# Kernel tuning notes

Hardware: AMD Instinct MI355X
Metric: run time of the kernel (lower is better)

Reference implementation:

```python
import jax, jax.numpy as jnp
import numpy as np

# SMPL kinematic tree (24 joints)
PARENTS = [-1, 0, 0, 0, 1, 2, 3, 4, 5, 6, 7, 8, 9, 9, 9, 12, 13, 14, 16, 17, 18, 19, 20, 21]
B, V, J, NB = 1024, 6890, 24, 10
POSE_BASIS = 9 * (J - 1)  # 207


def setup_inputs() -> dict:
    key = jax.random.key(0)
    ks = jax.random.split(key, 8)
    betas = jax.random.normal(ks[0], (B, NB), jnp.float32)
    global_rot = jax.random.normal(ks[1], (B, 1, 3, 3), jnp.float32)
    body_pose = jax.random.normal(ks[2], (B, J - 1, 3, 3), jnp.float32)
    v_template = jax.random.normal(ks[3], (V, 3), jnp.float32)
    shapedirs = jax.random.normal(ks[4], (V, 3, NB), jnp.float32) * 0.01
    posedirs = jax.random.normal(ks[5], (POSE_BASIS, V * 3), jnp.float32) * 0.01
    J_regressor = jax.random.uniform(ks[6], (J, V), jnp.float32) / V
    w = jax.random.uniform(ks[7], (V, J), jnp.float32)
    lbs_weights = w / w.sum(-1, keepdims=True)
    return dict(betas=betas, global_rot=global_rot, body_pose=body_pose,
                v_template=v_template, shapedirs=shapedirs, posedirs=posedirs,
                J_regressor=J_regressor, lbs_weights=lbs_weights)


def reference(betas, global_rot, body_pose, v_template, shapedirs, posedirs,
              J_regressor, lbs_weights):
    b = betas.shape[0]
    full_pose = jnp.concatenate([global_rot, body_pose], axis=1)  # [B,24,3,3]

    # shape blend shapes
    v_shaped = v_template + jnp.einsum('bl,vcl->bvc', betas, shapedirs)  # [B,V,3]
    Jt = jnp.einsum('jv,bvc->bjc', J_regressor, v_shaped)  # [B,24,3]

    # pose blend shapes (pose2rot=False: rotations given)
    eye3 = jnp.eye(3, dtype=betas.dtype)
    pose_feature = (full_pose[:, 1:] - eye3).reshape(b, POSE_BASIS)  # [B,207]
    v_posed = v_shaped + (pose_feature @ posedirs).reshape(b, V, 3)

    # forward kinematics along parent chain
    rel_joints = jnp.concatenate(
        [Jt[:, :1], Jt[:, 1:] - Jt[:, jnp.array(PARENTS[1:])]], axis=1)  # [B,24,3]
    top = jnp.concatenate([full_pose, rel_joints[..., None]], axis=-1)  # [B,24,3,4]
    bottom = jnp.broadcast_to(jnp.array([0., 0., 0., 1.], dtype=betas.dtype),
                              (b, J, 1, 4))
    T_local = jnp.concatenate([top, bottom], axis=-2)  # [B,24,4,4]

    chain = [T_local[:, 0]]
    for i in range(1, J):  # fixed small tree, sequential dependency
        chain.append(chain[PARENTS[i]] @ T_local[:, i])
    A = jnp.stack(chain, axis=1)  # [B,24,4,4]

    posed_joints = A[..., :3, 3]  # [B,24,3]
    # make transforms relative to rest-pose joints
    rel_t = posed_joints - jnp.einsum('bjmn,bjn->bjm', A[..., :3, :3], Jt)
    A_rel = A.at[..., :3, 3].set(rel_t)

    # linear blend skinning
    T = jnp.einsum('vj,bjmn->bvmn', lbs_weights, A_rel)  # [B,V,4,4]
    vertices = jnp.einsum('bvmn,bvn->bvm', T[..., :3, :3], v_posed) + T[..., :3, 3]
    return vertices, posed_joints
```

## Files before the change

### kernel.cpp

```cpp
#include <hip/hip_runtime.h>

#define BN 1024
#define NV 6890
#define NBETA 10
#define PB 207
#define N3 20670
#define NCOL 20736
#define NCHUNK 7
#define BT 32

typedef __bf16 bf16x8 __attribute__((ext_vector_type(8)));
typedef float  f32x4  __attribute__((ext_vector_type(4)));

__device__ __constant__ int c_par[24] = {-1,0,0,0,1,2,3,4,5,6,7,8,9,9,9,12,13,14,16,17,18,19,20,21};

__device__ inline unsigned short f2bf(float f) {
    unsigned u = __float_as_uint(f);
    u += 0x7fff + ((u >> 16) & 1);
    return (unsigned short)(u >> 16);
}

__global__ __launch_bounds__(256) void k_prep(const float* __restrict__ pd,
                                              const float* __restrict__ sd,
                                              const float* __restrict__ vtm,
                                              const float* __restrict__ Jr,
                                              const float* __restrict__ bpose,
                                              const float* __restrict__ betas,
                                              const float* __restrict__ w,
                                              unsigned short* __restrict__ ws_pdt,
                                              unsigned short* __restrict__ ws_pfb,
                                              unsigned short* __restrict__ ws_wb,
                                              float* __restrict__ ws_jsp)
{
    int blk = blockIdx.x;
    if (blk < 567) {
        int t = blk * 256 + threadIdx.x;
        int kc = t / NCOL;
        int col = t - kc * NCOL;
        bool cok = col < N3;
        unsigned short vals[40];
        #pragma unroll
        for (int kk = 0; kk < 32; kk++) {
            int gk = kc * 32 + kk;
            float val = 0.f;
            if (cok) {
                if (gk < PB)             val = pd[(size_t)gk * N3 + col];
                else if (gk < PB + 10)   val = sd[(size_t)col * NBETA + (gk - PB)];
                else if (gk == PB + 10)  val = vtm[col];
            }
            vals[kk] = f2bf(val);
        }
        #pragma unroll
        for (int kk = 32; kk < 40; kk++) vals[kk] = 0;
        uint4* dst = (uint4*)(ws_pdt + (size_t)t * 40);
        #pragma unroll
        for (int q = 0; q < 5; q++) {
            uint4 u;
            u.x = vals[q*8+0] | ((unsigned)vals[q*8+1] << 16);
            u.y = vals[q*8+2] | ((unsigned)vals[q*8+3] << 16);
            u.z = vals[q*8+4] | ((unsigned)vals[q*8+5] << 16);
            u.w = vals[q*8+6] | ((unsigned)vals[q*8+7] << 16);
            dst[q] = u;
        }
    } else if (blk < 799) {
        int e0 = (blk - 567) * 1024 + threadIdx.x * 4;
        unsigned short v4[4];
        #pragma unroll
        for (int r = 0; r < 4; r++) {
            int e = e0 + r;
            int b = e / 232, k = e - b * 232;
            float x = 0.f;
            if (k < PB) {
                x = bpose[(size_t)b * PB + k];
                int k9 = k % 9;
                if (k9 == 0 || k9 == 4 || k9 == 8) x -= 1.f;
            } else if (k < PB + 10) {
                x = betas[b * NBETA + (k - PB)];
            } else if (k == PB + 10) {
                x = 1.f;
            }
            v4[r] = f2bf(x);
        }
        uint2 u;
        u.x = v4[0] | ((unsigned)v4[1] << 16);
        u.y = v4[2] | ((unsigned)v4[3] << 16);
        *(uint2*)(ws_pfb + e0) = u;
    } else if (blk < 1069) {
        int e0 = (blk - 799) * 1024 + threadIdx.x * 4;
        unsigned short v4[4];
        #pragma unroll
        for (int r = 0; r < 4; r++) {
            int e = e0 + r;
            int v = e / 40, j = e - v * 40;
            float val = (j < 24 && v < NV) ? w[(size_t)v * 24 + j] : 0.f;
            v4[r] = f2bf(val);
        }
        uint2 u;
        u.x = v4[0] | ((unsigned)v4[1] << 16);
        u.y = v4[2] | ((unsigned)v4[3] << 16);
        *(uint2*)(ws_wb + e0) = u;
    } else {
        int b2 = blk - 1069;
        int jc = b2 >> 3;
        int seg = b2 & 7;
        int j = jc / 3, c = jc % 3;
        int v0 = seg * 862;
        int v1 = v0 + 862; if (v1 > NV) v1 = NV;

        float acc[11];
        #pragma unroll
        for (int l = 0; l < 11; l++) acc[l] = 0.f;

        for (int v = v0 + threadIdx.x; v < v1; v += 256) {
            float r = Jr[j * NV + v];
            acc[10] += r * vtm[v * 3 + c];
            const float* s = sd + (size_t)(v * 3 + c) * NBETA;
            #pragma unroll
            for (int l = 0; l < NBETA; l++) acc[l] += r * s[l];
        }

        __shared__ float red[4][11];
        int lane = threadIdx.x & 63, wv = threadIdx.x >> 6;
        #pragma unroll
        for (int l = 0; l < 11; l++) {
            float x = acc[l];
            x += __shfl_down(x, 32, 64);
            x += __shfl_down(x, 16, 64);
            x += __shfl_down(x, 8, 64);
            x += __shfl_down(x, 4, 64);
            x += __shfl_down(x, 2, 64);
            x += __shfl_down(x, 1, 64);
            if (lane == 0) red[wv][l] = x;
        }
        __syncthreads();
        if (threadIdx.x == 0) {
            #pragma unroll
            for (int l = 0; l < 11; l++)
                ws_jsp[((size_t)seg * 72 + jc) * 11 + l]
                    = red[0][l] + red[1][l] + red[2][l] + red[3][l];
        }
    }
}

__global__ __launch_bounds__(256) void k_chain(const float* __restrict__ betas,
                                               const float* __restrict__ grot,
                                               const float* __restrict__ bpose,
                                               const float* __restrict__ ws_jsp,
                                               unsigned short* __restrict__ ws_artb,
                                               float* __restrict__ pj)
{
    __shared__ float js_s[72 * 11];
    __shared__ float jt[16][72];
    __shared__ float tl[16][288];
    __shared__ float am[16][288];
    int tid = threadIdx.x;

    for (int e = tid; e < 72 * 11; e += 256) {
        float s = 0.f;
        #pragma unroll
        for (int seg = 0; seg < 8; seg++)
            s += ws_jsp[(size_t)seg * 792 + e];
        js_s[e] = s;
    }
    __syncthreads();

    int lb = tid >> 4;
    int e  = tid & 15;
    int b  = blockIdx.x * 16 + lb;

    for (int idx = e; idx < 72; idx += 16) {
        float acc = js_s[idx * 11 + 10];
        const float* be = betas + b * NBETA;
        #pragma unroll
        for (int l = 0; l < NBETA; l++) acc += be[l] * js_s[idx * 11 + l];
        jt[lb][idx] = acc;
    }
    __syncthreads();

    for (int idx = e; idx < 288; idx += 16) {
        int j = idx / 12, e12 = idx % 12, m = e12 >> 2, n = e12 & 3;
        float val;
        if (n < 3) {
            val = (j == 0) ? grot[(size_t)b * 9 + m * 3 + n]
                           : bpose[((size_t)b * 23 + (j - 1)) * 9 + m * 3 + n];
        } else {
            val = jt[lb][j * 3 + m];
            if (j > 0) val -= jt[lb][c_par[j] * 3 + m];
        }
        tl[lb][idx] = val;
    }
    __syncthreads();

    if (e < 12) am[lb][e] = tl[lb][e];
    for (int i = 1; i < 24; i++) {
        __syncthreads();
        if (e < 12) {
            int p = c_par[i];
            int m = e >> 2, n = e & 3;
            float val = am[lb][p*12 + m*4 + 0] * tl[lb][i*12 + 0 + n]
                      + am[lb][p*12 + m*4 + 1] * tl[lb][i*12 + 4 + n]
                      + am[lb][p*12 + m*4 + 2] * tl[lb][i*12 + 8 + n];
            if (n == 3) val += am[lb][p*12 + m*4 + 3];
            am[lb][i*12 + e] = val;
        }
    }
    __syncthreads();

    for (int idx = e; idx < 72; idx += 16) {
        int j = idx / 3, m = idx % 3;
        pj[(size_t)b * 72 + idx] = am[lb][j*12 + m*4 + 3];
    }
    for (int idx = e; idx < 480; idx += 16) {
        int col = idx / 40, j = idx - col * 40;
        float val = 0.f;
        if (j < 24) {
            int m = col >> 2, n = col & 3;
            if (n < 3) {
                val = am[lb][j*12 + col];
            } else {
                val = am[lb][j*12 + m*4 + 3]
                    - am[lb][j*12 + m*4 + 0] * jt[lb][j*3 + 0]
                    - am[lb][j*12 + m*4 + 1] * jt[lb][j*3 + 1]
                    - am[lb][j*12 + m*4 + 2] * jt[lb][j*3 + 2];
            }
        }
        ws_artb[(size_t)b * 480 + idx] = f2bf(val);
    }
}

__global__ __launch_bounds__(256, 6) void k_vert(const unsigned short* __restrict__ ws_pdt,
                                                 const unsigned short* __restrict__ ws_pfb,
                                                 const unsigned short* __restrict__ ws_wb,
                                                 const unsigned short* __restrict__ ws_artb,
                                                 float* __restrict__ out)
{
    const int lin = blockIdx.x + 32 * blockIdx.y;
    const int xcd = lin & 7;
    const int loc = lin >> 3;
    const int g_id = xcd * 432 + loc;
    const int bb = g_id & 31;
    const int vb = g_id >> 5;

    const int tid = threadIdx.x;
    const int wv = tid >> 6;
    const int lane = tid & 63;
    const int r16 = lane & 15;
    const int half8 = (lane >> 4) * 8;

    __shared__ __align__(16) float disp_l[32 * 196];

    const unsigned short* pfbase = ws_pfb + (size_t)(bb * BT) * 232;
    const unsigned short* pB0 = ws_pdt + ((size_t)vb * 192 + wv * 48 + r16) * 40 + half8;

    bf16x8 a0 = *(const bf16x8*)(pfbase + r16 * 232 + half8);
    bf16x8 a1 = *(const bf16x8*)(pfbase + (16 + r16) * 232 + half8);
    bf16x8 b0 = *(const bf16x8*)(pB0);
    bf16x8 b1 = *(const bf16x8*)(pB0 + 640);
    bf16x8 b2 = *(const bf16x8*)(pB0 + 1280);

    f32x4 acc[2][3];
    #pragma unroll
    for (int mt = 0; mt < 2; mt++)
        #pragma unroll
        for (int t = 0; t < 3; t++)
            acc[mt][t] = (f32x4){0.f, 0.f, 0.f, 0.f};

    #pragma unroll
    for (int kc = 0; kc < NCHUNK; kc++) {
        bf16x8 a0n, a1n, b0n, b1n, b2n;
        if (kc < NCHUNK - 1) {
            const unsigned short* pn = pB0 + (size_t)(kc + 1) * NCOL * 40;
            b0n = *(const bf16x8*)(pn);
            b1n = *(const bf16x8*)(pn + 640);
            b2n = *(const bf16x8*)(pn + 1280);
            a0n = *(const bf16x8*)(pfbase + r16 * 232 + (kc + 1) * 32 + half8);
            a1n = *(const bf16x8*)(pfbase + (16 + r16) * 232 + (kc + 1) * 32 + half8);
        }
        acc[0][0] = __builtin_amdgcn_mfma_f32_16x16x32_bf16(a0, b0, acc[0][0], 0, 0, 0);
        acc[1][0] = __builtin_amdgcn_mfma_f32_16x16x32_bf16(a1, b0, acc[1][0], 0, 0, 0);
        acc[0][1] = __builtin_amdgcn_mfma_f32_16x16x32_bf16(a0, b1, acc[0][1], 0, 0, 0);
        acc[1][1] = __builtin_amdgcn_mfma_f32_16x16x32_bf16(a1, b1, acc[1][1], 0, 0, 0);
        acc[0][2] = __builtin_amdgcn_mfma_f32_16x16x32_bf16(a0, b2, acc[0][2], 0, 0, 0);
        acc[1][2] = __builtin_amdgcn_mfma_f32_16x16x32_bf16(a1, b2, acc[1][2], 0, 0, 0);
        if (kc < NCHUNK - 1) { a0 = a0n; a1 = a1n; b0 = b0n; b1 = b1n; b2 = b2n; }
    }

    #pragma unroll
    for (int mt = 0; mt < 2; mt++) {
        #pragma unroll
        for (int t = 0; t < 3; t++) {
            int col = wv * 48 + t * 16 + r16;
            int brow = mt * 16 + (lane >> 4) * 4;
            #pragma unroll
            for (int r = 0; r < 4; r++)
                disp_l[(brow + r) * 196 + col] = acc[mt][t][r];
        }
    }
    __syncthreads();

    bf16x8 aw = *(const bf16x8*)(ws_wb + (size_t)(vb * 64 + wv * 16 + r16) * 40 + half8);

    const int gq = lane >> 4;
    const int v16 = wv * 16 + r16;
    const int vg = vb * 64 + v16;
    int bl[3], mm[3];
    #pragma unroll
    for (int t = 0; t < 3; t++) {
        int q = 4 * t + gq;
        bl[t] = (q * 11) >> 5;
        mm[t] = q - 3 * bl[t];
    }

    const unsigned short* pArt = ws_artb + (size_t)(bb * BT) * 480 + (size_t)r16 * 40 + half8;

    bf16x8 c0 = *(const bf16x8*)(pArt);
    bf16x8 c1 = *(const bf16x8*)(pArt + 640);
    bf16x8 c2 = *(const bf16x8*)(pArt + 1280);

    #pragma unroll
    for (int sub = 0; sub < 8; sub++) {
        bf16x8 c0n, c1n, c2n;
        if (sub < 7) {
            const unsigned short* pn = pArt + (size_t)(sub + 1) * 1920;
            c0n = *(const bf16x8*)(pn);
            c1n = *(const bf16x8*)(pn + 640);
            c2n = *(const bf16x8*)(pn + 1280);
        }
        f32x4 z = (f32x4){0.f, 0.f, 0.f, 0.f};
        f32x4 t0 = __builtin_amdgcn_mfma_f32_16x16x32_bf16(c0, aw, z, 0, 0, 0);
        f32x4 t1 = __builtin_amdgcn_mfma_f32_16x16x32_bf16(c1, aw, z, 0, 0, 0);
        f32x4 t2 = __builtin_amdgcn_mfma_f32_16x16x32_bf16(c2, aw, z, 0, 0, 0);

        #pragma unroll
        for (int t = 0; t < 3; t++) {
            f32x4 tt = (t == 0) ? t0 : (t == 1) ? t1 : t2;
            int row = sub * 4 + bl[t];
            const float* d = disp_l + row * 196 + v16 * 3;
            float x = d[0], y = d[1], zz = d[2];
            float p = tt[0] * x + tt[1] * y + tt[2] * zz + tt[3];
            if (vg < NV)
                out[(size_t)(bb * BT + row) * N3 + (size_t)vg * 3 + mm[t]] = p;
        }
        if (sub < 7) { c0 = c0n; c1 = c1n; c2 = c2n; }
    }
}

extern "C" void kernel_launch(void* const* d_in, const int* in_sizes, int n_in,
                              void* d_out, int out_size, void* d_ws, size_t ws_size,
                              hipStream_t stream) {
    const float* betas = (const float*)d_in[0];
    const float* grot  = (const float*)d_in[1];
    const float* bpose = (const float*)d_in[2];
    const float* vtm   = (const float*)d_in[3];
    const float* sd    = (const float*)d_in[4];
    const float* pd    = (const float*)d_in[5];
    const float* Jr    = (const float*)d_in[6];
    const float* w     = (const float*)d_in[7];
    float* out = (float*)d_out;

    char* ws = (char*)d_ws;
    unsigned short* ws_pdt  = (unsigned short*)(ws);
    unsigned short* ws_pfb  = (unsigned short*)(ws + 11612160);
    unsigned short* ws_wb   = (unsigned short*)(ws + 12087296);
    float*          ws_jsp  = (float*)         (ws + 12640256);
    unsigned short* ws_artb = (unsigned short*)(ws + 12665600);

    k_prep<<<1645, 256, 0, stream>>>(pd, sd, vtm, Jr, bpose, betas, w,
                                     ws_pdt, ws_pfb, ws_wb, ws_jsp);
    k_chain<<<BN / 16, 256, 0, stream>>>(betas, grot, bpose, ws_jsp, ws_artb,
                                         out + (size_t)BN * N3);
    k_vert<<<dim3(32, 108), 256, 0, stream>>>(ws_pdt, ws_pfb, ws_wb, ws_artb, out);
}
```

Baseline: 185.6 us.

## Stage pose features in LDS via async DMA and re-split skinning across waves

The per-batch pose-feature tile is now copied into shared memory with global_load_lds DMA and read from LDS in the K loop, replacing per-wave global loads and register double-buffering. The skinning epilogue is re-partitioned so each wave handles two batch sub-blocks across all four vertex groups, rather than one vertex group across all eight sub-blocks. Occupancy hint drops from 6 to 4 blocks per CU to accommodate the larger LDS footprint. This aims to cut redundant global traffic for the A operand and the artb tiles, but adds a barrier and lowers occupancy. Output stores now come from each wave covering 64 vertices, which may change the coalescing pattern.

```diff
diff --git a/kernel.cpp b/kernel.cpp
--- a/kernel.cpp
+++ b/kernel.cpp
@@ -18,6 +18,12 @@
     unsigned u = __float_as_uint(f);
     u += 0x7fff + ((u >> 16) & 1);
     return (unsigned short)(u >> 16);
+}
+
+__device__ inline void dma16(const void* g, void* l) {
+    __builtin_amdgcn_global_load_lds(
+        (const __attribute__((address_space(1))) unsigned int*)g,
+        (__attribute__((address_space(3))) unsigned int*)l, 16, 0, 0);
 }
 
 __global__ __launch_bounds__(256) void k_prep(const float* __restrict__ pd,
@@ -228,7 +234,7 @@
     }
 }
 
-__global__ __launch_bounds__(256, 6) void k_vert(const unsigned short* __restrict__ ws_pdt,
+__global__ __launch_bounds__(256, 4) void k_vert(const unsigned short* __restrict__ ws_pdt,
                                                  const unsigned short* __restrict__ ws_pfb,
                                                  const unsigned short* __restrict__ ws_wb,
                                                  const unsigned short* __restrict__ ws_artb,
@@ -247,13 +253,19 @@
     const int r16 = lane & 15;
     const int half8 = (lane >> 4) * 8;
 
-    __shared__ __align__(16) float disp_l[32 * 196];
-
-    const unsigned short* pfbase = ws_pfb + (size_t)(bb * BT) * 232;
+    __shared__ __align__(16) unsigned char smem[40448];
+    float*          disp_l = (float*)smem;
+    unsigned short* pfb_l  = (unsigned short*)(smem + 25088);
+
+    {
+        const unsigned short* srcF = ws_pfb + (size_t)(bb * BT) * 232;
+        for (int i = wv; i < 14; i += 4)
+            dma16((const char*)srcF + i * 1024 + lane * 16, (char*)pfb_l + i * 1024);
+        if (wv == 2 && lane < 32)
+            dma16((const char*)srcF + 14 * 1024 + lane * 16, (char*)pfb_l + 14 * 1024);
+    }
+
     const unsigned short* pB0 = ws_pdt + ((size_t)vb * 192 + wv * 48 + r16) * 40 + half8;
-
-    bf16x8 a0 = *(const bf16x8*)(pfbase + r16 * 232 + half8);
-    bf16x8 a1 = *(const bf16x8*)(pfbase + (16 + r16) * 232 + half8);
     bf16x8 b0 = *(const bf16x8*)(pB0);
     bf16x8 b1 = *(const bf16x8*)(pB0 + 640);
     bf16x8 b2 = *(const bf16x8*)(pB0 + 1280);
@@ -265,16 +277,18 @@
         for (int t = 0; t < 3; t++)
             acc[mt][t] = (f32x4){0.f, 0.f, 0.f, 0.f};
 
+    __syncthreads();
+
     #pragma unroll
     for (int kc = 0; kc < NCHUNK; kc++) {
-        bf16x8 a0n, a1n, b0n, b1n, b2n;
+        bf16x8 a0 = *(const bf16x8*)(pfb_l + r16 * 232 + kc * 32 + half8);
+        bf16x8 a1 = *(const bf16x8*)(pfb_l + (16 + r16) * 232 + kc * 32 + half8);
+        bf16x8 b0n, b1n, b2n;
         if (kc < NCHUNK - 1) {
             const unsigned short* pn = pB0 + (size_t)(kc + 1) * NCOL * 40;
             b0n = *(const bf16x8*)(pn);
             b1n = *(const bf16x8*)(pn + 640);
             b2n = *(const bf16x8*)(pn + 1280);
-            a0n = *(const bf16x8*)(pfbase + r16 * 232 + (kc + 1) * 32 + half8);
-            a1n = *(const bf16x8*)(pfbase + (16 + r16) * 232 + (kc + 1) * 32 + half8);
         }
         acc[0][0] = __builtin_amdgcn_mfma_f32_16x16x32_bf16(a0, b0, acc[0][0], 0, 0, 0);
         acc[1][0] = __builtin_amdgcn_mfma_f32_16x16x32_bf16(a1, b0, acc[1][0], 0, 0, 0);
@@ -282,7 +296,7 @@
         acc[1][1] = __builtin_amdgcn_mfma_f32_16x16x32_bf16(a1, b1, acc[1][1], 0, 0, 0);
         acc[0][2] = __builtin_amdgcn_mfma_f32_16x16x32_bf16(a0, b2, acc[0][2], 0, 0, 0);
         acc[1][2] = __builtin_amdgcn_mfma_f32_16x16x32_bf16(a1, b2, acc[1][2], 0, 0, 0);
-        if (kc < NCHUNK - 1) { a0 = a0n; a1 = a1n; b0 = b0n; b1 = b1n; b2 = b2n; }
+        if (kc < NCHUNK - 1) { b0 = b0n; b1 = b1n; b2 = b2n; }
     }
 
     #pragma unroll
@@ -298,11 +312,7 @@
     }
     __syncthreads();
 
-    bf16x8 aw = *(const bf16x8*)(ws_wb + (size_t)(vb * 64 + wv * 16 + r16) * 40 + half8);
-
     const int gq = lane >> 4;
-    const int v16 = wv * 16 + r16;
-    const int vg = vb * 64 + v16;
     int bl[3], mm[3];
     #pragma unroll
     for (int t = 0; t < 3; t++) {
@@ -311,37 +321,49 @@
         mm[t] = q - 3 * bl[t];
     }
 
-    const unsigned short* pArt = ws_artb + (size_t)(bb * BT) * 480 + (size_t)r16 * 40 + half8;
-
-    bf16x8 c0 = *(const bf16x8*)(pArt);
-    bf16x8 c1 = *(const bf16x8*)(pArt + 640);
-    bf16x8 c2 = *(const bf16x8*)(pArt + 1280);
-
-    #pragma unroll
-    for (int sub = 0; sub < 8; sub++) {
+    bf16x8 aw[4];
+    #pragma unroll
+    for (int vg = 0; vg < 4; vg++)
+        aw[vg] = *(const bf16x8*)(ws_wb + (size_t)(vb * 64 + vg * 16 + r16) * 40 + half8);
+
+    const unsigned short* pArt0 = ws_artb + (size_t)(bb * BT) * 480 + (size_t)r16 * 40 + half8;
+
+    const unsigned short* pc = pArt0 + (size_t)wv * 1920;
+    bf16x8 c0 = *(const bf16x8*)(pc);
+    bf16x8 c1 = *(const bf16x8*)(pc + 640);
+    bf16x8 c2 = *(const bf16x8*)(pc + 1280);
+
+    #pragma unroll
+    for (int h = 0; h < 2; h++) {
+        const int sub = wv + h * 4;
         bf16x8 c0n, c1n, c2n;
-        if (sub < 7) {
-            const unsigned short* pn = pArt + (size_t)(sub + 1) * 1920;
+        if (h == 0) {
+            const unsigned short* pn = pArt0 + (size_t)(wv + 4) * 1920;
             c0n = *(const bf16x8*)(pn);
             c1n = *(const bf16x8*)(pn + 640);
             c2n = *(const bf16x8*)(pn + 1280);
         }
-        f32x4 z = (f32x4){0.f, 0.f, 0.f, 0.f};
-        f32x4 t0 = __builtin_amdgcn_mfma_f32_16x16x32_bf16(c0, aw, z, 0, 0, 0);
-        f32x4 t1 = __builtin_amdgcn_mfma_f32_16x16x32_bf16(c1, aw, z, 0, 0, 0);
-        f32x4 t2 = __builtin_amdgcn_mfma_f32_16x16x32_bf16(c2, aw, z, 0, 0, 0);
-
-        #pragma unroll
-        for (int t = 0; t < 3; t++) {
-            f32x4 tt = (t == 0) ? t0 : (t == 1) ? t1 : t2;
-            int row = sub * 4 + bl[t];
-            const float* d = disp_l + row * 196 + v16 * 3;
-            float x = d[0], y = d[1], zz = d[2];
-            float p = tt[0] * x + tt[1] * y + tt[2] * zz + tt[3];
-            if (vg < NV)
-                out[(size_t)(bb * BT + row) * N3 + (size_t)vg * 3 + mm[t]] = p;
-        }
-        if (sub < 7) { c0 = c0n; c1 = c1n; c2 = c2n; }
+        #pragma unroll
+        for (int vg = 0; vg < 4; vg++) {
+            f32x4 z = (f32x4){0.f, 0.f, 0.f, 0.f};
+            f32x4 t0 = __builtin_amdgcn_mfma_f32_16x16x32_bf16(c0, aw[vg], z, 0, 0, 0);
+            f32x4 t1 = __builtin_amdgcn_mfma_f32_16x16x32_bf16(c1, aw[vg], z, 0, 0, 0);
+            f32x4 t2 = __builtin_amdgcn_mfma_f32_16x16x32_bf16(c2, aw[vg], z, 0, 0, 0);
+
+            const int v16 = vg * 16 + r16;
+            const int vg_glob = vb * 64 + v16;
+            #pragma unroll
+            for (int t = 0; t < 3; t++) {
+                f32x4 tt = (t == 0) ? t0 : (t == 1) ? t1 : t2;
+                int row = sub * 4 + bl[t];
+                const float* d = disp_l + row * 196 + v16 * 3;
+                float x = d[0], y = d[1], zz = d[2];
+                float p = tt[0] * x + tt[1] * y + tt[2] * zz + tt[3];
+                if (vg_glob < NV)
+                    out[(size_t)(bb * BT + row) * N3 + (size_t)vg_glob * 3 + mm[t]] = p;
+            }
+        }
+        if (h == 0) { c0 = c0n; c1 = c1n; c2 = c2n; }
     }
 }
 
```

Result: faster. 171.1 us (-7.8%).
